# Optimization experiments

Hardware: AMD Instinct MI355X
Metric: run time of the kernel (lower is better)

Reference implementation:

```python
import jax, jax.numpy as jnp
import numpy as np

N_NODES = 100000
N_EDGES = 1000000
IN_F, HID_F, OUT_F = 128, 128, 16


def setup_inputs() -> dict:
    key = jax.random.key(0)
    ks = jax.random.split(key, 8)
    x = jax.random.normal(ks[0], (N_NODES, IN_F), dtype=jnp.float32)
    src = jax.random.randint(ks[1], (N_EDGES,), 0, N_NODES, dtype=jnp.int64)
    dst = jax.random.randint(ks[2], (N_EDGES,), 0, N_NODES, dtype=jnp.int64)
    s = 1.0 / np.sqrt(HID_F)
    W1 = jax.random.normal(ks[3], (IN_F, HID_F), dtype=jnp.float32) * s
    W2 = jax.random.normal(ks[4], (HID_F, HID_F), dtype=jnp.float32) * s
    W3 = jax.random.normal(ks[5], (HID_F, HID_F), dtype=jnp.float32) * s
    W4 = jax.random.normal(ks[6], (HID_F, HID_F), dtype=jnp.float32) * s
    W5 = jax.random.normal(ks[7], (HID_F, OUT_F), dtype=jnp.float32) * s
    return {
        "x": x, "src": src, "dst": dst,
        "W1": W1, "b1": jnp.zeros((HID_F,), jnp.float32),
        "W2": W2, "b2": jnp.zeros((HID_F,), jnp.float32),
        "W3": W3, "b3": jnp.zeros((HID_F,), jnp.float32),
        "W4": W4, "b4": jnp.zeros((HID_F,), jnp.float32),
        "W5": W5, "b5": jnp.zeros((OUT_F,), jnp.float32),
    }


def reference(x, src, dst, W1, b1, W2, b2, W3, b3, W4, b4, W5, b5):
    N = x.shape[0]
    # in-degree per destination node (static graph, computed once)
    deg = jax.ops.segment_sum(jnp.ones_like(dst, dtype=x.dtype), dst, num_segments=N)
    inv = (1.0 / (deg + 1.0))[:, None]  # gcn aggregator normalizer: 1/(deg_in+1)

    def sage_gcn(h, W, b):
        # h_neigh[v] = (h[v] + sum_{u->v} h[u]) / (deg_in(v)+1); then linear
        agg = (h + jax.ops.segment_sum(h[src], dst, num_segments=N)) * inv
        return agg @ W + b

    h = jax.nn.relu(sage_gcn(x, W1, b1))
    h = jax.nn.relu(sage_gcn(h, W2, b2))
    h = jax.nn.relu(sage_gcn(h, W3, b3))
    h = jax.nn.relu(sage_gcn(h, W4, b4))
    h = sage_gcn(h, W5, b5)
    return jax.nn.log_softmax(h, axis=-1)
```

## Files before the change

### kernel.cpp

```cpp
#include <hip/hip_runtime.h>
#include <hip/hip_bf16.h>

#define NNODES 100000
#define NP (NNODES + 8)
#define NEDGES 1000000
#define HID 128
#define OUTF 16
#define NB 16
#define NBKT (NNODES / NB)
#define BCAP 81920
#define KB 64
#define BZT 1024
#define DB2 32
#define NBINS (NB * DB2)
#define NSL 4

typedef __attribute__((ext_vector_type(8))) short short8;
typedef __attribute__((ext_vector_type(4))) float floatx4;
typedef __attribute__((ext_vector_type(4))) unsigned int uintx4;
typedef unsigned int uint32;
typedef unsigned long long ull;
typedef unsigned short ushort16;

__device__ __forceinline__ float blo(uint32 u) { return __uint_as_float(u << 16); }
__device__ __forceinline__ float bhi(uint32 u) { return __uint_as_float(u & 0xffff0000u); }
__device__ __forceinline__ ushort16 f2b(float f) {
    __hip_bfloat16 h = __float2bfloat16(f);
    return *reinterpret_cast<ushort16*>(&h);
}
__device__ __forceinline__ uint32 pack2(float a, float b) {
    return (uint32)f2b(a) | ((uint32)f2b(b) << 16);
}


__global__ __launch_bounds__(BZT) void bucketize(const int* __restrict__ src,
                                                 const int* __restrict__ dst,
                                                 int* __restrict__ bcursor,
                                                 ull* __restrict__ stage, int E) {
    __shared__ int cnt[NB], lbase[NB], gbase[NB];
    __shared__ int2 buf[BZT];
    __shared__ unsigned char bb[BZT];
    int t = threadIdx.x;
    int e0 = blockIdx.x * BZT;
    int e = e0 + t;
    if (t < NB) cnt[t] = 0;
    __syncthreads();
    int s = 0, d = 0, b = 0, r = 0;
    bool valid = e < E;
    if (valid) {
        s = src[e];
        d = dst[e];
        b = d / NBKT;
        r = atomicAdd(&cnt[b], 1);
    }
    __syncthreads();
    if (t == 0) {
        int run = 0;
        for (int i = 0; i < NB; i++) { lbase[i] = run; run += cnt[i]; }
    }
    __syncthreads();
    if (valid) {
        int p = lbase[b] + r;
        buf[p] = make_int2(s, d);
        bb[p] = (unsigned char)b;
    }
    if (t < NB) gbase[t] = atomicAdd(&bcursor[t], cnt[t]);
    __syncthreads();
    int nvalid = min(BZT, E - e0);
    if (t < nvalid) {
        int b2 = bb[t];
        int2 sd = buf[t];
        int pos = gbase[b2] + (t - lbase[b2]);
        if (pos < BCAP) {
            ull val = (ull)(unsigned)sd.x | ((ull)(unsigned)sd.y << 32);
            __builtin_nontemporal_store(val, &stage[(size_t)b2 * BCAP + pos]);
        }
    }
}


__global__ __launch_bounds__(256) void count_rank(const ull* __restrict__ stage,
                                                  const int* __restrict__ bcursor,
                                                  int* __restrict__ counts,
                                                  int* __restrict__ rnk) {
    int blk = blockIdx.x;
    int b = (blk & 7) + 8 * ((blk >> 3) & 1);
    int slot = blk >> 4;
    int cntb = min(bcursor[b], BCAP);
    int per = (cntb + KB - 1) / KB;
    int s0 = slot * per;
    int s1 = min(s0 + per, cntb);
    const ull* st = stage + (size_t)b * BCAP;
    int* rk = rnk + (size_t)b * BCAP;
    for (int i = s0 + threadIdx.x; i < s1; i += 256) {
        ull v = st[i];
        int d = (int)(unsigned)(v >> 32);
        rk[i] = atomicAdd(&counts[d], 1);
    }
}


__global__ __launch_bounds__(256) void fill2(const ull* __restrict__ stage,
                                             const int* __restrict__ rnk,
                                             const int* __restrict__ bcursor,
                                             const int* __restrict__ perm,
                                             const int* __restrict__ offs,
                                             int* __restrict__ csr) {
    int blk = blockIdx.x;
    int b = (blk & 7) + 8 * ((blk >> 3) & 1);
    int slot = blk >> 4;
    int cntb = min(bcursor[b], BCAP);
    int per = (cntb + KB - 1) / KB;
    int s0 = slot * per;
    int s1 = min(s0 + per, cntb);
    const ull* st = stage + (size_t)b * BCAP;
    const int* rk = rnk + (size_t)b * BCAP;
    for (int i = s0 + threadIdx.x; i < s1; i += 256) {
        ull v = st[i];
        int s = (int)(v & 0xffffffffu);
        int d = (int)(unsigned)(v >> 32);
        int pd = perm[d];
        csr[offs[pd] + rk[i]] = perm[s];
    }
}


__global__ __launch_bounds__(256) void binhist(const int* __restrict__ counts,
                                               int* __restrict__ bins, int N) {
    __shared__ int h[NBINS];
    int t = threadIdx.x;
    for (int k = t; k < NBINS; k += 256) h[k] = 0;
    __syncthreads();
    int i = blockIdx.x * 256 + t;
    if (i < N) {
        int bi = i / NBKT;
        int db = min((counts[i] + 7) >> 3, DB2 - 1);
        atomicAdd(&h[bi * DB2 + db], 1);
    }
    __syncthreads();
    for (int k = t; k < NBINS; k += 256)
        if (h[k] > 0) atomicAdd(&bins[k], h[k]);
}

__global__ void binscan(int* __restrict__ bins) {
    if (threadIdx.x == 0) {
        int run = 0;
        for (int i = 0; i < NBINS; i++) {
            int c = bins[i];
            bins[i] = run;
            run += c;
        }
    }
}

__global__ __launch_bounds__(256) void dsort2(const int* __restrict__ counts,
                                              int* __restrict__ bins,
                                              int* __restrict__ perm,
                                              int* __restrict__ iperm,
                                              int* __restrict__ cnts_s, int N) {
    __shared__ int h[NBINS], lb[NBINS];
    int t = threadIdx.x;
    for (int k = t; k < NBINS; k += 256) h[k] = 0;
    __syncthreads();
    int i = blockIdx.x * 256 + t;
    int c = 0, idx = 0, r = 0;
    bool valid = i < N;
    if (valid) {
        c = counts[i];
        int bi = i / NBKT;
        idx = bi * DB2 + min((c + 7) >> 3, DB2 - 1);
        r = atomicAdd(&h[idx], 1);
    }
    __syncthreads();
    for (int k = t; k < NBINS; k += 256)
        lb[k] = (h[k] > 0) ? atomicAdd(&bins[k], h[k]) : 0;
    __syncthreads();
    if (valid) {
        int p = lb[idx] + r;
        perm[i] = p;
        iperm[p] = i;
        cnts_s[p] = c;
    }
}

__global__ void scan1(const int* __restrict__ cnts_s, int* __restrict__ offs,
                      int* __restrict__ bsum, int N) {
    __shared__ int tmp[256];
    int t = threadIdx.x;
    int i = blockIdx.x * 256 + t;
    int v = (i < N) ? ((cnts_s[i] + 7) & ~7) : 0;
    tmp[t] = v;
    __syncthreads();
    for (int d = 1; d < 256; d <<= 1) {
        int add = (t >= d) ? tmp[t - d] : 0;
        __syncthreads();
        tmp[t] += add;
        __syncthreads();
    }
    if (i < N) offs[i] = tmp[t] - v;
    if (t == 255) bsum[blockIdx.x] = tmp[255];
}

__global__ void scan2(int* __restrict__ bsum, int nb) {
    __shared__ int tmp[512];
    int t = threadIdx.x;
    int v = (t < nb) ? bsum[t] : 0;
    tmp[t] = v;
    __syncthreads();
    for (int d = 1; d < 512; d <<= 1) {
        int add = (t >= d) ? tmp[t - d] : 0;
        __syncthreads();
        tmp[t] += add;
        __syncthreads();
    }
    if (t < nb) bsum[t] = tmp[t] - v;
}

__global__ void scan3(int* __restrict__ offs, const int* __restrict__ bsum,
                      const int* __restrict__ cnts_s, float* __restrict__ invs,
                      int* __restrict__ csr, int N) {
    int i = blockIdx.x * 256 + threadIdx.x;
    if (i < N) {
        int o = offs[i] + bsum[blockIdx.x];
        offs[i] = o;
        int c = cnts_s[i];
        invs[i] = 1.0f / (float)(c + 1);
        int c8 = (c + 7) & ~7;
        for (int k = c; k < c8; k++) csr[o + k] = NNODES;
    }
}


__global__ void pack_all(const float* __restrict__ W1, const float* __restrict__ W2,
                         const float* __restrict__ W3, const float* __restrict__ W4,
                         ushort16* __restrict__ Wp1, ushort16* __restrict__ Wp2,
                         ushort16* __restrict__ Wp3, ushort16* __restrict__ Wp4,
                         uint32* __restrict__ zb, uint32* __restrict__ hb,
                         uint32* __restrict__ z16b) {
    int blk = blockIdx.x;
    int lane = threadIdx.x;
    if (blk < 128) {
        int w = blk >> 5, b = blk & 31;
        const float* W = w == 0 ? W1 : w == 1 ? W2 : w == 2 ? W3 : W4;
        ushort16* Wp = w == 0 ? Wp1 : w == 1 ? Wp2 : w == 2 ? Wp3 : Wp4;
        int nt = b >> 2, ks = b & 3;
        int n = nt * 16 + (lane & 15);
        int kbase = ks * 32 + ((lane >> 4) << 3);
        ushort16 tmp[8];
#pragma unroll
        for (int i = 0; i < 8; i++) tmp[i] = f2b(W[(size_t)(kbase + i) * HID + n]);
        *(uint4*)&Wp[((size_t)b * 64 + lane) * 8] = *(uint4*)tmp;
    } else {
        for (int i = lane; i < 4 * 8 * 16; i += 64) {
            int s = i >> 7, rem = i & 127, r = rem >> 4, k = rem & 15;
            zb[((size_t)s * NP + NNODES + r) * 16 + k] = 0;
            hb[((size_t)s * NP + NNODES + r) * 16 + k] = 0;
        }
        for (int i = lane; i < 64; i += 64)
            z16b[(size_t)(NNODES + (i >> 3)) * 8 + (i & 7)] = 0;
    }
}


template <int AF32>
__global__ __launch_bounds__(256) void gemm_mfma(const void* __restrict__ Av,
                                                 const int* __restrict__ iperm,
                                                 const ushort16* __restrict__ Wp,
                                                 ushort16* __restrict__ Z, int M) {
    __shared__ __align__(16) ushort16 Wl[32 * 64 * 8];
    int t = threadIdx.x;
    const uint4* wp4 = (const uint4*)Wp;
    uint4* wl4 = (uint4*)Wl;
#pragma unroll
    for (int p = 0; p < 8; p++) wl4[t + p * 256] = wp4[t + p * 256];
    __syncthreads();

    int wv = t >> 6, lane = t & 63;
    int kb = (lane >> 4) << 3;
    int c4 = (lane >> 4) << 2;

    for (int rt = 0; rt < 4; rt++) {
        int row = blockIdx.x * 256 + rt * 64 + wv * 16 + (lane & 15);
        int rowc = min(row, M - 1);

        short8 a[4];
        if (AF32) {
            const float* A = (const float*)Av;
            int orig = iperm[rowc];
#pragma unroll
            for (int ks = 0; ks < 4; ks++) {
                const float* p = A + (size_t)orig * HID + ks * 32 + kb;
                floatx4 lo = *(const floatx4*)p;
                floatx4 hi = *(const floatx4*)(p + 4);
                union { short8 s; ushort16 u[8]; } cv;
                cv.u[0] = f2b(lo.x); cv.u[1] = f2b(lo.y); cv.u[2] = f2b(lo.z); cv.u[3] = f2b(lo.w);
                cv.u[4] = f2b(hi.x); cv.u[5] = f2b(hi.y); cv.u[6] = f2b(hi.z); cv.u[7] = f2b(hi.w);
                a[ks] = cv.s;
            }
        } else {
            const ushort16* A = (const ushort16*)Av;
#pragma unroll
            for (int ks = 0; ks < 4; ks++)
                a[ks] = *(const short8*)(A + ((size_t)ks * NP + rowc) * 32 + kb);
        }

        floatx4 acc[8];
#pragma unroll
        for (int nt = 0; nt < 8; nt++) acc[nt] = (floatx4){0.f, 0.f, 0.f, 0.f};

#pragma unroll
        for (int nt = 0; nt < 8; nt++) {
#pragma unroll
            for (int ks = 0; ks < 4; ks++) {
                short8 w = *(const short8*)&Wl[(size_t)(((nt << 2) | ks) * 64 + lane) * 8];
                acc[nt] = __builtin_amdgcn_mfma_f32_16x16x32_bf16(w, a[ks], acc[nt], 0, 0, 0);
            }
        }

        if (row < M) {
#pragma unroll
            for (int nt = 0; nt < 8; nt++) {
                int col = nt * 16 + c4;
                int sl = col >> 5, off = col & 31;
                union { ushort16 u[4]; uint2 v; } pk;
                pk.u[0] = f2b(acc[nt][0]);
                pk.u[1] = f2b(acc[nt][1]);
                pk.u[2] = f2b(acc[nt][2]);
                pk.u[3] = f2b(acc[nt][3]);
                *(uint2*)&Z[((size_t)sl * NP + row) * 32 + off] = pk.v;
            }
        }
    }
}


#define ACCN(acc0, acc1, acc2, acc3, g)                \
    {                                                  \
        acc0.x += blo((g).x); acc0.y += bhi((g).x);    \
        acc1.x += blo((g).y); acc1.y += bhi((g).y);    \
        acc2.x += blo((g).z); acc2.y += bhi((g).z);    \
        acc3.x += blo((g).w); acc3.y += bhi((g).w);    \
    }

__global__ __launch_bounds__(256) void agg_sliced(const uint32* __restrict__ Z,
                                                  const int* __restrict__ offs,
                                                  const int* __restrict__ cnts_s,
                                                  const int* __restrict__ csr,
                                                  const float* __restrict__ invs,
                                                  const float* __restrict__ bias,
                                                  uint32* __restrict__ H, int N) {
    int s = blockIdx.x & 3;
    int chunk = blockIdx.x >> 2;
    int t = threadIdx.x;
    int l = t & 3;
    int p = chunk * 64 + (t >> 2);
    bool act = p < N;
    int pc = act ? p : N - 1;
    const uint4* Zs = (const uint4*)(Z + (size_t)s * NP * 16);
    uint4* Hs = (uint4*)(H + (size_t)s * NP * 16);

    int beg = offs[pc];
    int cnt8 = (cnts_s[pc] + 7) & ~7;
    float sc = invs[pc];

    uint4 sv = Zs[(size_t)pc * 4 + l];
    float2 acc0 = make_float2(blo(sv.x), bhi(sv.x));
    float2 acc1 = make_float2(blo(sv.y), bhi(sv.y));
    float2 acc2 = make_float2(blo(sv.z), bhi(sv.z));
    float2 acc3 = make_float2(blo(sv.w), bhi(sv.w));

    for (int j = 0; j < cnt8; j += 8) {
        int4 ia = *(const int4*)&csr[beg + j];
        int4 ib = *(const int4*)&csr[beg + j + 4];
        uint4 g[8];
        g[0] = Zs[(size_t)ia.x * 4 + l];
        g[1] = Zs[(size_t)ia.y * 4 + l];
        g[2] = Zs[(size_t)ia.z * 4 + l];
        g[3] = Zs[(size_t)ia.w * 4 + l];
        g[4] = Zs[(size_t)ib.x * 4 + l];
        g[5] = Zs[(size_t)ib.y * 4 + l];
        g[6] = Zs[(size_t)ib.z * 4 + l];
        g[7] = Zs[(size_t)ib.w * 4 + l];
#pragma unroll
        for (int q = 0; q < 8; q++) ACCN(acc0, acc1, acc2, acc3, g[q]);
    }

    const float* bp = bias + s * 32 + l * 8;
    floatx4 b01 = *(const floatx4*)bp;
    floatx4 b23 = *(const floatx4*)(bp + 4);
    uintx4 o;
    o.x = pack2(fmaxf(acc0.x * sc + b01.x, 0.f), fmaxf(acc0.y * sc + b01.y, 0.f));
    o.y = pack2(fmaxf(acc1.x * sc + b01.z, 0.f), fmaxf(acc1.y * sc + b01.w, 0.f));
    o.z = pack2(fmaxf(acc2.x * sc + b23.x, 0.f), fmaxf(acc2.y * sc + b23.y, 0.f));
    o.w = pack2(fmaxf(acc3.x * sc + b23.z, 0.f), fmaxf(acc3.y * sc + b23.w, 0.f));
    if (act) __builtin_nontemporal_store(o, (uintx4*)&Hs[(size_t)p * 4 + l]);
}


__global__ __launch_bounds__(256) void gemm16(const uint32* __restrict__ A,
                                              const float* __restrict__ W5,
                                              uint32* __restrict__ Z16, int M) {
    __shared__ float Ws[HID * OUTF];
    int t = threadIdx.x;
    for (int i = t; i < HID * OUTF; i += 256) Ws[i] = W5[i];
    __syncthreads();
    int gid = blockIdx.x * 256 + t;
    int r = gid >> 3, cp = gid & 7;
    if (r >= M) return;
    float a0 = 0.f, a1 = 0.f;
#pragma unroll
    for (int s4 = 0; s4 < 4; s4++) {
        const uint32* ar = A + ((size_t)s4 * NP + r) * 16;
#pragma unroll
        for (int k = 0; k < 16; k++) {
            uint32 u = ar[k];
            float f0 = blo(u), f1 = bhi(u);
            a0 += f0 * Ws[(s4 * 32 + 2 * k) * OUTF + 2 * cp] +
                  f1 * Ws[(s4 * 32 + 2 * k + 1) * OUTF + 2 * cp];
            a1 += f0 * Ws[(s4 * 32 + 2 * k) * OUTF + 2 * cp + 1] +
                  f1 * Ws[(s4 * 32 + 2 * k + 1) * OUTF + 2 * cp + 1];
        }
    }
    Z16[(size_t)r * 8 + cp] = pack2(a0, a1);
}


__global__ __launch_bounds__(256) void agg16_lsm(const uint32* __restrict__ Z16,
                                                 const int* __restrict__ offs,
                                                 const int* __restrict__ cnts_s,
                                                 const int* __restrict__ csr,
                                                 const float* __restrict__ invs,
                                                 const int* __restrict__ iperm,
                                                 const float* __restrict__ b5,
                                                 float* __restrict__ out, int N) {
    int t = threadIdx.x;
    int l = t & 1;
    int p = blockIdx.x * 128 + (t >> 1);
    bool act = p < N;
    int pc = act ? p : N - 1;
    const uint4* Zs = (const uint4*)Z16;

    uint4 sv = Zs[(size_t)pc * 2 + l];
    float2 acc0 = make_float2(blo(sv.x), bhi(sv.x));
    float2 acc1 = make_float2(blo(sv.y), bhi(sv.y));
    float2 acc2 = make_float2(blo(sv.z), bhi(sv.z));
    float2 acc3 = make_float2(blo(sv.w), bhi(sv.w));

    int beg = offs[pc];
    int cnt8 = (cnts_s[pc] + 7) & ~7;
    for (int j = 0; j < cnt8; j += 8) {
        int4 ia = *(const int4*)&csr[beg + j];
        int4 ib = *(const int4*)&csr[beg + j + 4];
        uint4 g[8];
        g[0] = Zs[(size_t)ia.x * 2 + l];
        g[1] = Zs[(size_t)ia.y * 2 + l];
        g[2] = Zs[(size_t)ia.z * 2 + l];
        g[3] = Zs[(size_t)ia.w * 2 + l];
        g[4] = Zs[(size_t)ib.x * 2 + l];
        g[5] = Zs[(size_t)ib.y * 2 + l];
        g[6] = Zs[(size_t)ib.z * 2 + l];
        g[7] = Zs[(size_t)ib.w * 2 + l];
#pragma unroll
        for (int q = 0; q < 8; q++) ACCN(acc0, acc1, acc2, acc3, g[q]);
    }

    float sc = invs[pc];
    const float* bp = b5 + l * 8;
    floatx4 b01 = *(const floatx4*)bp;
    floatx4 b23 = *(const floatx4*)(bp + 4);
    float val[8];
    val[0] = acc0.x * sc + b01.x; val[1] = acc0.y * sc + b01.y;
    val[2] = acc1.x * sc + b01.z; val[3] = acc1.y * sc + b01.w;
    val[4] = acc2.x * sc + b23.x; val[5] = acc2.y * sc + b23.y;
    val[6] = acc3.x * sc + b23.z; val[7] = acc3.y * sc + b23.w;
    float mm = val[0];
#pragma unroll
    for (int k = 1; k < 8; k++) mm = fmaxf(mm, val[k]);
    mm = fmaxf(mm, __shfl_xor(mm, 1, 64));
    float ss = 0.f;
#pragma unroll
    for (int k = 0; k < 8; k++) ss += expf(val[k] - mm);
    ss += __shfl_xor(ss, 1, 64);
    float ls = mm + logf(ss);
    if (act) {
        int ov = iperm[p];
        float4 o0 = make_float4(val[0] - ls, val[1] - ls, val[2] - ls, val[3] - ls);
        float4 o1 = make_float4(val[4] - ls, val[5] - ls, val[6] - ls, val[7] - ls);
        float* op = out + (size_t)ov * OUTF + l * 8;
        *(float4*)op = o0;
        *(float4*)(op + 4) = o1;
    }
}


extern "C" void kernel_launch(void* const* d_in, const int* in_sizes, int n_in,
                              void* d_out, int out_size, void* d_ws, size_t ws_size,
                              hipStream_t stream) {
    const float* x   = (const float*)d_in[0];
    const int*   src = (const int*)d_in[1];
    const int*   dst = (const int*)d_in[2];
    const float* W1 = (const float*)d_in[3];
    const float* b1 = (const float*)d_in[4];
    const float* W2 = (const float*)d_in[5];
    const float* b2 = (const float*)d_in[6];
    const float* W3 = (const float*)d_in[7];
    const float* b3 = (const float*)d_in[8];
    const float* W4 = (const float*)d_in[9];
    const float* b4 = (const float*)d_in[10];
    const float* W5 = (const float*)d_in[11];
    const float* b5 = (const float*)d_in[12];

    char* ws = (char*)d_ws;
    size_t off = 0;
    auto alloc = [&](size_t bytes) {
        void* p = ws + off;
        off = (off + bytes + 255) & ~(size_t)255;
        return p;
    };
    const size_t CSR_ELEMS = (size_t)NEDGES + 7 * (size_t)NNODES + 64;
    ushort16* zb   = (ushort16*)alloc((size_t)NSL * NP * 32 * 2);
    ushort16* hb   = (ushort16*)alloc((size_t)NSL * NP * 32 * 2);
    uint32*   z16b = (uint32*)alloc((size_t)NP * OUTF * 2);
    int*      counts = (int*)alloc((size_t)NNODES * 4);
    int*      cnts_s = (int*)alloc((size_t)NNODES * 4);
    int*      perm   = (int*)alloc((size_t)NNODES * 4);
    int*      iperm  = (int*)alloc((size_t)NNODES * 4);
    float*    invs   = (float*)alloc((size_t)NNODES * 4);
    int*      offs   = (int*)alloc((size_t)(NNODES + 1) * 4);
    int*      bsum   = (int*)alloc(512 * 4);
    int*      csr    = (int*)alloc(CSR_ELEMS * 4);
    ull*      stage  = (ull*)alloc((size_t)NB * BCAP * 8);
    int*      rnk    = (int*)alloc((size_t)NB * BCAP * 4);
    int*      bcursor = (int*)alloc((NB + NBINS) * 4);
    int*      bins   = bcursor + NB;
    ushort16* Wp1 = (ushort16*)alloc((size_t)HID * HID * 2);
    ushort16* Wp2 = (ushort16*)alloc((size_t)HID * HID * 2);
    ushort16* Wp3 = (ushort16*)alloc((size_t)HID * HID * 2);
    ushort16* Wp4 = (ushort16*)alloc((size_t)HID * HID * 2);
    (void)ws_size; (void)in_sizes; (void)n_in; (void)out_size;

    const int N = NNODES, E = NEDGES;
    int nb = (N + 255) / 256;

    hipMemsetAsync(counts, 0, (size_t)N * 4, stream);
    hipMemsetAsync(bcursor, 0, (NB + NBINS) * 4, stream);
    bucketize<<<(E + BZT - 1) / BZT, BZT, 0, stream>>>(src, dst, bcursor, stage, E);
    count_rank<<<NB * KB, 256, 0, stream>>>(stage, bcursor, counts, rnk);
    binhist<<<nb, 256, 0, stream>>>(counts, bins, N);
    binscan<<<1, 64, 0, stream>>>(bins);
    dsort2<<<nb, 256, 0, stream>>>(counts, bins, perm, iperm, cnts_s, N);
    scan1<<<nb, 256, 0, stream>>>(cnts_s, offs, bsum, N);
    scan2<<<1, 512, 0, stream>>>(bsum, nb);
    scan3<<<nb, 256, 0, stream>>>(offs, bsum, cnts_s, invs, csr, N);
    fill2<<<NB * KB, 256, 0, stream>>>(stage, rnk, bcursor, perm, offs, csr);
    pack_all<<<129, 64, 0, stream>>>(W1, W2, W3, W4, Wp1, Wp2, Wp3, Wp4,
                                     (uint32*)zb, (uint32*)hb, z16b);

    int gemmGrid = (N + 255) / 256;
    int aggGrid  = NSL * ((N + 63) / 64);
    int agg16Grid = (N + 127) / 128;

    gemm_mfma<1><<<gemmGrid, 256, 0, stream>>>((const void*)x, iperm, Wp1, zb, N);
    agg_sliced<<<aggGrid, 256, 0, stream>>>((const uint32*)zb, offs, cnts_s, csr, invs, b1,
                                            (uint32*)hb, N);

    gemm_mfma<0><<<gemmGrid, 256, 0, stream>>>((const void*)hb, nullptr, Wp2, zb, N);
    agg_sliced<<<aggGrid, 256, 0, stream>>>((const uint32*)zb, offs, cnts_s, csr, invs, b2,
                                            (uint32*)hb, N);

    gemm_mfma<0><<<gemmGrid, 256, 0, stream>>>((const void*)hb, nullptr, Wp3, zb, N);
    agg_sliced<<<aggGrid, 256, 0, stream>>>((const uint32*)zb, offs, cnts_s, csr, invs, b3,
                                            (uint32*)hb, N);

    gemm_mfma<0><<<gemmGrid, 256, 0, stream>>>((const void*)hb, nullptr, Wp4, zb, N);
    agg_sliced<<<aggGrid, 256, 0, stream>>>((const uint32*)zb, offs, cnts_s, csr, invs, b4,
                                            (uint32*)hb, N);

    gemm16<<<(N * 8 + 255) / 256, 256, 0, stream>>>((const uint32*)hb, W5, z16b, N);
    agg16_lsm<<<agg16Grid, 256, 0, stream>>>(z16b, offs, cnts_s, csr, invs, iperm, b5,
                                             (float*)d_out, N);
}
```

Baseline: 371.9 us.

## Drop degree-sorted node permutation and aggregate in original node order

Removes the degree-binning node permutation (binhist, binscan, dsort2) and all perm/iperm indirection, so the CSR, GEMMs and aggregation kernels work on nodes in their original order. This saves three preprocessing launches, the indirect gathers through iperm in the first GEMM, and the scatter through iperm in the output. In exchange, warps in the aggregation kernels no longer see nodes of similar degree grouped together, which may raise load imbalance and divergence in the per-node neighbor loops.

```diff
diff --git a/kernel.cpp b/kernel.cpp
--- a/kernel.cpp
+++ b/kernel.cpp
@@ -11,8 +11,6 @@
 #define BCAP 81920
 #define KB 64
 #define BZT 1024
-#define DB2 32
-#define NBINS (NB * DB2)
 #define NSL 4
 
 typedef __attribute__((ext_vector_type(8))) short short8;
@@ -103,7 +101,6 @@
 __global__ __launch_bounds__(256) void fill2(const ull* __restrict__ stage,
                                              const int* __restrict__ rnk,
                                              const int* __restrict__ bcursor,
-                                             const int* __restrict__ perm,
                                              const int* __restrict__ offs,
                                              int* __restrict__ csr) {
     int blk = blockIdx.x;
@@ -119,76 +116,16 @@
         ull v = st[i];
         int s = (int)(v & 0xffffffffu);
         int d = (int)(unsigned)(v >> 32);
-        int pd = perm[d];
-        csr[offs[pd] + rk[i]] = perm[s];
-    }
-}
-
-
-__global__ __launch_bounds__(256) void binhist(const int* __restrict__ counts,
-                                               int* __restrict__ bins, int N) {
-    __shared__ int h[NBINS];
-    int t = threadIdx.x;
-    for (int k = t; k < NBINS; k += 256) h[k] = 0;
-    __syncthreads();
-    int i = blockIdx.x * 256 + t;
-    if (i < N) {
-        int bi = i / NBKT;
-        int db = min((counts[i] + 7) >> 3, DB2 - 1);
-        atomicAdd(&h[bi * DB2 + db], 1);
-    }
-    __syncthreads();
-    for (int k = t; k < NBINS; k += 256)
-        if (h[k] > 0) atomicAdd(&bins[k], h[k]);
-}
-
-__global__ void binscan(int* __restrict__ bins) {
-    if (threadIdx.x == 0) {
-        int run = 0;
-        for (int i = 0; i < NBINS; i++) {
-            int c = bins[i];
-            bins[i] = run;
-            run += c;
-        }
-    }
-}
-
-__global__ __launch_bounds__(256) void dsort2(const int* __restrict__ counts,
-                                              int* __restrict__ bins,
-                                              int* __restrict__ perm,
-                                              int* __restrict__ iperm,
-                                              int* __restrict__ cnts_s, int N) {
-    __shared__ int h[NBINS], lb[NBINS];
-    int t = threadIdx.x;
-    for (int k = t; k < NBINS; k += 256) h[k] = 0;
-    __syncthreads();
-    int i = blockIdx.x * 256 + t;
-    int c = 0, idx = 0, r = 0;
-    bool valid = i < N;
-    if (valid) {
-        c = counts[i];
-        int bi = i / NBKT;
-        idx = bi * DB2 + min((c + 7) >> 3, DB2 - 1);
-        r = atomicAdd(&h[idx], 1);
-    }
-    __syncthreads();
-    for (int k = t; k < NBINS; k += 256)
-        lb[k] = (h[k] > 0) ? atomicAdd(&bins[k], h[k]) : 0;
-    __syncthreads();
-    if (valid) {
-        int p = lb[idx] + r;
-        perm[i] = p;
-        iperm[p] = i;
-        cnts_s[p] = c;
-    }
-}
-
-__global__ void scan1(const int* __restrict__ cnts_s, int* __restrict__ offs,
+        csr[offs[d] + rk[i]] = s;
+    }
+}
+
+__global__ void scan1(const int* __restrict__ counts, int* __restrict__ offs,
                       int* __restrict__ bsum, int N) {
     __shared__ int tmp[256];
     int t = threadIdx.x;
     int i = blockIdx.x * 256 + t;
-    int v = (i < N) ? ((cnts_s[i] + 7) & ~7) : 0;
+    int v = (i < N) ? ((counts[i] + 7) & ~7) : 0;
     tmp[t] = v;
     __syncthreads();
     for (int d = 1; d < 256; d <<= 1) {
@@ -217,13 +154,13 @@
 }
 
 __global__ void scan3(int* __restrict__ offs, const int* __restrict__ bsum,
-                      const int* __restrict__ cnts_s, float* __restrict__ invs,
+                      const int* __restrict__ counts, float* __restrict__ invs,
                       int* __restrict__ csr, int N) {
     int i = blockIdx.x * 256 + threadIdx.x;
     if (i < N) {
         int o = offs[i] + bsum[blockIdx.x];
         offs[i] = o;
-        int c = cnts_s[i];
+        int c = counts[i];
         invs[i] = 1.0f / (float)(c + 1);
         int c8 = (c + 7) & ~7;
         for (int k = c; k < c8; k++) csr[o + k] = NNODES;
@@ -264,7 +201,6 @@
 
 template <int AF32>
 __global__ __launch_bounds__(256) void gemm_mfma(const void* __restrict__ Av,
-                                                 const int* __restrict__ iperm,
                                                  const ushort16* __restrict__ Wp,
                                                  ushort16* __restrict__ Z, int M) {
     __shared__ __align__(16) ushort16 Wl[32 * 64 * 8];
@@ -286,10 +222,9 @@
         short8 a[4];
         if (AF32) {
             const float* A = (const float*)Av;
-            int orig = iperm[rowc];
 #pragma unroll
             for (int ks = 0; ks < 4; ks++) {
-                const float* p = A + (size_t)orig * HID + ks * 32 + kb;
+                const float* p = A + (size_t)rowc * HID + ks * 32 + kb;
                 floatx4 lo = *(const floatx4*)p;
                 floatx4 hi = *(const floatx4*)(p + 4);
                 union { short8 s; ushort16 u[8]; } cv;
@@ -321,13 +256,13 @@
 #pragma unroll
             for (int nt = 0; nt < 8; nt++) {
                 int col = nt * 16 + c4;
-                int sl = col >> 5, off = col & 31;
+                int sl = col >> 5, off2 = col & 31;
                 union { ushort16 u[4]; uint2 v; } pk;
                 pk.u[0] = f2b(acc[nt][0]);
                 pk.u[1] = f2b(acc[nt][1]);
                 pk.u[2] = f2b(acc[nt][2]);
                 pk.u[3] = f2b(acc[nt][3]);
-                *(uint2*)&Z[((size_t)sl * NP + row) * 32 + off] = pk.v;
+                *(uint2*)&Z[((size_t)sl * NP + row) * 32 + off2] = pk.v;
             }
         }
     }
@@ -344,7 +279,7 @@
 
 __global__ __launch_bounds__(256) void agg_sliced(const uint32* __restrict__ Z,
                                                   const int* __restrict__ offs,
-                                                  const int* __restrict__ cnts_s,
+                                                  const int* __restrict__ counts,
                                                   const int* __restrict__ csr,
                                                   const float* __restrict__ invs,
                                                   const float* __restrict__ bias,
@@ -360,7 +295,7 @@
     uint4* Hs = (uint4*)(H + (size_t)s * NP * 16);
 
     int beg = offs[pc];
-    int cnt8 = (cnts_s[pc] + 7) & ~7;
+    int cnt8 = (counts[pc] + 7) & ~7;
     float sc = invs[pc];
 
     uint4 sv = Zs[(size_t)pc * 4 + l];
@@ -427,10 +362,9 @@
 
 __global__ __launch_bounds__(256) void agg16_lsm(const uint32* __restrict__ Z16,
                                                  const int* __restrict__ offs,
-                                                 const int* __restrict__ cnts_s,
+                                                 const int* __restrict__ counts,
                                                  const int* __restrict__ csr,
                                                  const float* __restrict__ invs,
-                                                 const int* __restrict__ iperm,
                                                  const float* __restrict__ b5,
                                                  float* __restrict__ out, int N) {
     int t = threadIdx.x;
@@ -447,7 +381,7 @@
     float2 acc3 = make_float2(blo(sv.w), bhi(sv.w));
 
     int beg = offs[pc];
-    int cnt8 = (cnts_s[pc] + 7) & ~7;
+    int cnt8 = (counts[pc] + 7) & ~7;
     for (int j = 0; j < cnt8; j += 8) {
         int4 ia = *(const int4*)&csr[beg + j];
         int4 ib = *(const int4*)&csr[beg + j + 4];
@@ -483,10 +417,9 @@
     ss += __shfl_xor(ss, 1, 64);
     float ls = mm + logf(ss);
     if (act) {
-        int ov = iperm[p];
         float4 o0 = make_float4(val[0] - ls, val[1] - ls, val[2] - ls, val[3] - ls);
         float4 o1 = make_float4(val[4] - ls, val[5] - ls, val[6] - ls, val[7] - ls);
-        float* op = out + (size_t)ov * OUTF + l * 8;
+        float* op = out + (size_t)p * OUTF + l * 8;
         *(float4*)op = o0;
         *(float4*)(op + 4) = o1;
     }
@@ -521,18 +454,14 @@
     ushort16* zb   = (ushort16*)alloc((size_t)NSL * NP * 32 * 2);
     ushort16* hb   = (ushort16*)alloc((size_t)NSL * NP * 32 * 2);
     uint32*   z16b = (uint32*)alloc((size_t)NP * OUTF * 2);
-    int*      counts = (int*)alloc((size_t)NNODES * 4);
-    int*      cnts_s = (int*)alloc((size_t)NNODES * 4);
-    int*      perm   = (int*)alloc((size_t)NNODES * 4);
-    int*      iperm  = (int*)alloc((size_t)NNODES * 4);
+    int*      counts = (int*)alloc((size_t)(NNODES + NB) * 4);
+    int*      bcursor = counts + NNODES;
     float*    invs   = (float*)alloc((size_t)NNODES * 4);
     int*      offs   = (int*)alloc((size_t)(NNODES + 1) * 4);
     int*      bsum   = (int*)alloc(512 * 4);
     int*      csr    = (int*)alloc(CSR_ELEMS * 4);
     ull*      stage  = (ull*)alloc((size_t)NB * BCAP * 8);
     int*      rnk    = (int*)alloc((size_t)NB * BCAP * 4);
-    int*      bcursor = (int*)alloc((NB + NBINS) * 4);
-    int*      bins   = bcursor + NB;
     ushort16* Wp1 = (ushort16*)alloc((size_t)HID * HID * 2);
     ushort16* Wp2 = (ushort16*)alloc((size_t)HID * HID * 2);
     ushort16* Wp3 = (ushort16*)alloc((size_t)HID * HID * 2);
@@ -542,17 +471,13 @@
     const int N = NNODES, E = NEDGES;
     int nb = (N + 255) / 256;
 
-    hipMemsetAsync(counts, 0, (size_t)N * 4, stream);
-    hipMemsetAsync(bcursor, 0, (NB + NBINS) * 4, stream);
+    hipMemsetAsync(counts, 0, (size_t)(NNODES + NB) * 4, stream);
     bucketize<<<(E + BZT - 1) / BZT, BZT, 0, stream>>>(src, dst, bcursor, stage, E);
     count_rank<<<NB * KB, 256, 0, stream>>>(stage, bcursor, counts, rnk);
-    binhist<<<nb, 256, 0, stream>>>(counts, bins, N);
-    binscan<<<1, 64, 0, stream>>>(bins);
-    dsort2<<<nb, 256, 0, stream>>>(counts, bins, perm, iperm, cnts_s, N);
-    scan1<<<nb, 256, 0, stream>>>(cnts_s, offs, bsum, N);
+    scan1<<<nb, 256, 0, stream>>>(counts, offs, bsum, N);
     scan2<<<1, 512, 0, stream>>>(bsum, nb);
-    scan3<<<nb, 256, 0, stream>>>(offs, bsum, cnts_s, invs, csr, N);
-    fill2<<<NB * KB, 256, 0, stream>>>(stage, rnk, bcursor, perm, offs, csr);
+    scan3<<<nb, 256, 0, stream>>>(offs, bsum, counts, invs, csr, N);
+    fill2<<<NB * KB, 256, 0, stream>>>(stage, rnk, bcursor, offs, csr);
     pack_all<<<129, 64, 0, stream>>>(W1, W2, W3, W4, Wp1, Wp2, Wp3, Wp4,
                                      (uint32*)zb, (uint32*)hb, z16b);
 
@@ -560,23 +485,23 @@
     int aggGrid  = NSL * ((N + 63) / 64);
     int agg16Grid = (N + 127) / 128;
 
-    gemm_mfma<1><<<gemmGrid, 256, 0, stream>>>((const void*)x, iperm, Wp1, zb, N);
-    agg_sliced<<<aggGrid, 256, 0, stream>>>((const uint32*)zb, offs, cnts_s, csr, invs, b1,
+    gemm_mfma<1><<<gemmGrid, 256, 0, stream>>>((const void*)x, Wp1, zb, N);
+    agg_sliced<<<aggGrid, 256, 0, stream>>>((const uint32*)zb, offs, counts, csr, invs, b1,
                                             (uint32*)hb, N);
 
-    gemm_mfma<0><<<gemmGrid, 256, 0, stream>>>((const void*)hb, nullptr, Wp2, zb, N);
-    agg_sliced<<<aggGrid, 256, 0, stream>>>((const uint32*)zb, offs, cnts_s, csr, invs, b2,
+    gemm_mfma<0><<<gemmGrid, 256, 0, stream>>>((const void*)hb, Wp2, zb, N);
+    agg_sliced<<<aggGrid, 256, 0, stream>>>((const uint32*)zb, offs, counts, csr, invs, b2,
                                             (uint32*)hb, N);
 
-    gemm_mfma<0><<<gemmGrid, 256, 0, stream>>>((const void*)hb, nullptr, Wp3, zb, N);
-    agg_sliced<<<aggGrid, 256, 0, stream>>>((const uint32*)zb, offs, cnts_s, csr, invs, b3,
+    gemm_mfma<0><<<gemmGrid, 256, 0, stream>>>((const void*)hb, Wp3, zb, N);
+    agg_sliced<<<aggGrid, 256, 0, stream>>>((const uint32*)zb, offs, counts, csr, invs, b3,
                                             (uint32*)hb, N);
 
-    gemm_mfma<0><<<gemmGrid, 256, 0, stream>>>((const void*)hb, nullptr, Wp4, zb, N);
-    agg_sliced<<<aggGrid, 256, 0, stream>>>((const uint32*)zb, offs, cnts_s, csr, invs, b4,
+    gemm_mfma<0><<<gemmGrid, 256, 0, stream>>>((const void*)hb, Wp4, zb, N);
+    agg_sliced<<<aggGrid, 256, 0, stream>>>((const uint32*)zb, offs, counts, csr, invs, b4,
                                             (uint32*)hb, N);
 
     gemm16<<<(N * 8 + 255) / 256, 256, 0, stream>>>((const uint32*)hb, W5, z16b, N);
-    agg16_lsm<<<agg16Grid, 256, 0, stream>>>(z16b, offs, cnts_s, csr, invs, iperm, b5,
+    agg16_lsm<<<agg16Grid, 256, 0, stream>>>(z16b, offs, counts, csr, invs, b5,
                                              (float*)d_out, N);
 }
```

After: 342.6 us. 1.09x faster.
